# Kernel optimization log

Hardware: AMD Instinct MI355X
Metric: run time of the kernel (lower is better)

## Reference

```python
import jax, jax.numpy as jnp
import numpy as np

N = 100000
E = 1600000
F_IN = 128
HID = 64
N_CLASS = 40
NEG_SLOPE = 0.2


def setup_inputs() -> dict:
    key = jax.random.key(0)
    ks = jax.random.split(key, 16)
    s = lambda *sh: 1.0 / np.sqrt(sh[0])
    inp = {
        "x": jax.random.normal(ks[0], (N, F_IN), dtype=jnp.float32),
        "edge_index": jax.random.randint(ks[1], (2, E), 0, N, dtype=jnp.int64),
        "W1": jax.random.normal(ks[2], (F_IN, HID), jnp.float32) * s(F_IN),
        "b1": jnp.zeros((HID,), jnp.float32),
        "Wc0": jax.random.normal(ks[3], (HID, HID), jnp.float32) * s(HID),
        "att_src0": jax.random.normal(ks[4], (HID,), jnp.float32) * s(HID),
        "att_dst0": jax.random.normal(ks[5], (HID,), jnp.float32) * s(HID),
        "bias0": jnp.zeros((HID,), jnp.float32),
        "Wc1": jax.random.normal(ks[6], (HID, HID), jnp.float32) * s(HID),
        "att_src1": jax.random.normal(ks[7], (HID,), jnp.float32) * s(HID),
        "att_dst1": jax.random.normal(ks[8], (HID,), jnp.float32) * s(HID),
        "bias1": jnp.zeros((HID,), jnp.float32),
        "W2": jax.random.normal(ks[9], (HID, N_CLASS), jnp.float32) * s(HID),
        "b2": jnp.zeros((N_CLASS,), jnp.float32),
    }
    return inp


def gat_conv(x, src, dst, W, att_src, att_dst, bias):
    # x: [N, Fin]; src/dst: [E'] (self-loops already appended)
    h = x @ W                                   # [N, Fout]
    a_s = h @ att_src                           # [N]
    a_d = h @ att_dst                           # [N]
    e = jax.nn.leaky_relu(a_s[src] + a_d[dst], NEG_SLOPE)   # [E']
    # segment softmax over edges grouped by destination node
    e_max = jax.ops.segment_max(e, dst, num_segments=N)     # every node has a self-loop
    ex = jnp.exp(e - e_max[dst])
    denom = jax.ops.segment_sum(ex, dst, num_segments=N)
    alpha = ex / (denom[dst] + 1e-16)                        # [E']
    out = jax.ops.segment_sum(h[src] * alpha[:, None], dst, num_segments=N)
    return out + bias


def reference(x, edge_index, W1, b1, Wc0, att_src0, att_dst0, bias0,
              Wc1, att_src1, att_dst1, bias1, W2, b2):
    # eval mode: dropout_adj and feature dropout are identity
    loop = jnp.arange(N, dtype=edge_index.dtype)
    src = jnp.concatenate([edge_index[0], loop])
    dst = jnp.concatenate([edge_index[1], loop])

    h = jax.nn.relu(x @ W1 + b1)
    h = gat_conv(h, src, dst, Wc0, att_src0, att_dst0, bias0)
    h = jax.nn.relu(h)
    h = gat_conv(h, src, dst, Wc1, att_src1, att_dst1, bias1)
    logits = h @ W2 + b2
    return jax.nn.log_softmax(logits, axis=-1)
```

## Files before the change

### kernel.cpp

```cpp
#include <hip/hip_runtime.h>

#define N_NODES 100000
#define N_EDGES 1600000
#define F_IN    128
#define HID     64
#define N_CLASS 40
#define NEG_SLOPE 0.2f
#define ET (N_EDGES + N_NODES)
#define ROW_BLOCKS ((N_NODES + 63) / 64)

#define NCB   7
#define CAP1  294912
#define BPC   144
#define NFB   782
#define CAPF  2624
#define NT1   ((ET + 2047) / 2048)

typedef __attribute__((ext_vector_type(8))) short bf16x8;
typedef __attribute__((ext_vector_type(4))) float f32x4;

__device__ __forceinline__ unsigned int f2bf(float f) {
    unsigned int u = __float_as_uint(f);
    return (u + 0x7fffu + ((u >> 16) & 1u)) >> 16;
}

__global__ __launch_bounds__(256) void k_prepw(const float* __restrict__ W1,
        const float* __restrict__ Wc0, const float* __restrict__ Wc1,
        unsigned short* __restrict__ Wt1, unsigned short* __restrict__ Wtc0,
        unsigned short* __restrict__ Wtc1) {
    int t = threadIdx.x;
    for (int i = t; i < F_IN * HID; i += 256) {
        int k = i >> 6, n = i & 63;
        Wt1[n * F_IN + k] = (unsigned short)f2bf(W1[i]);
    }
    for (int i = t; i < HID * HID; i += 256) {
        int k = i >> 6, n = i & 63;
        Wtc0[n * HID + k] = (unsigned short)f2bf(Wc0[i]);
        Wtc1[n * HID + k] = (unsigned short)f2bf(Wc1[i]);
    }
}

__global__ __launch_bounds__(256) void k_lin1(const float* __restrict__ x,
        const unsigned short* __restrict__ Wt1, const float* __restrict__ b1,
        unsigned short* __restrict__ h0b) {
    __shared__ float xs[4][16 * 68];
    int t = threadIdx.x;
    int lane = t & 63, w = t >> 6;
    int quad = lane >> 4, lr = lane & 15;
    int rowg0 = blockIdx.x * 64 + w * 16;

    bf16x8 bfr[4][4];
    #pragma unroll
    for (int kc = 0; kc < 4; ++kc)
        #pragma unroll
        for (int nt = 0; nt < 4; ++nt)
            bfr[kc][nt] = *(const bf16x8*)(Wt1 + (nt * 16 + lr) * F_IN
                                           + kc * 32 + quad * 8);
    f32x4 zero = {0.f, 0.f, 0.f, 0.f};
    f32x4 acc[4] = {zero, zero, zero, zero};

    int arow = rowg0 + lr; if (arow >= N_NODES) arow = N_NODES - 1;
    const float* ab = x + (size_t)arow * F_IN;
    #pragma unroll
    for (int kc = 0; kc < 4; ++kc) {
        const float* ap = ab + kc * 32 + quad * 8;
        float4 a0 = *(const float4*)ap;
        float4 a1 = *(const float4*)(ap + 4);
        union { bf16x8 v; unsigned int u[4]; } af;
        af.u[0] = f2bf(a0.x) | (f2bf(a0.y) << 16);
        af.u[1] = f2bf(a0.z) | (f2bf(a0.w) << 16);
        af.u[2] = f2bf(a1.x) | (f2bf(a1.y) << 16);
        af.u[3] = f2bf(a1.z) | (f2bf(a1.w) << 16);
        #pragma unroll
        for (int nt = 0; nt < 4; ++nt)
            acc[nt] = __builtin_amdgcn_mfma_f32_16x16x32_bf16(
                          af.v, bfr[kc][nt], acc[nt], 0, 0, 0);
    }
    #pragma unroll
    for (int nt = 0; nt < 4; ++nt) {
        float bv = b1[nt * 16 + lr];
        #pragma unroll
        for (int reg = 0; reg < 4; ++reg)
            xs[w][(quad * 4 + reg) * 68 + nt * 16 + lr] =
                fmaxf(acc[nt][reg] + bv, 0.f);
    }
    __syncthreads();
    #pragma unroll
    for (int j = 0; j < 2; ++j) {
        int task = j * 64 + lane;
        int r = task >> 3, g = task & 7;
        int grow = blockIdx.x * 64 + w * 16 + r;
        if (grow < N_NODES) {
            const float* p = xs[w] + r * 68 + g * 8;
            uint4 u;
            u.x = f2bf(p[0]) | (f2bf(p[1]) << 16);
            u.y = f2bf(p[2]) | (f2bf(p[3]) << 16);
            u.z = f2bf(p[4]) | (f2bf(p[5]) << 16);
            u.w = f2bf(p[6]) | (f2bf(p[7]) << 16);
            *(uint4*)(h0b + (size_t)grow * HID + g * 8) = u;
        }
    }
}

__global__ __launch_bounds__(256) void k_gemm_att(
        const unsigned short* __restrict__ hin,
        const unsigned short* __restrict__ Wt,
        const float* __restrict__ att_s, const float* __restrict__ att_d,
        unsigned short* __restrict__ hb, float* __restrict__ as_,
        float* __restrict__ ad_) {
    __shared__ float xs[4][16 * 68];
    int t = threadIdx.x;
    int lane = t & 63, w = t >> 6;
    int quad = lane >> 4, lr = lane & 15;
    int rowg0 = blockIdx.x * 64 + w * 16;

    bf16x8 bfr[2][4];
    #pragma unroll
    for (int kc = 0; kc < 2; ++kc)
        #pragma unroll
        for (int nt = 0; nt < 4; ++nt)
            bfr[kc][nt] = *(const bf16x8*)(Wt + (nt * 16 + lr) * HID
                                           + kc * 32 + quad * 8);
    f32x4 zero = {0.f, 0.f, 0.f, 0.f};
    f32x4 acc[4] = {zero, zero, zero, zero};

    int arow = rowg0 + lr; if (arow >= N_NODES) arow = N_NODES - 1;
    #pragma unroll
    for (int kc = 0; kc < 2; ++kc) {
        bf16x8 af = *(const bf16x8*)(hin + (size_t)arow * HID
                                     + kc * 32 + quad * 8);
        #pragma unroll
        for (int nt = 0; nt < 4; ++nt)
            acc[nt] = __builtin_amdgcn_mfma_f32_16x16x32_bf16(
                          af, bfr[kc][nt], acc[nt], 0, 0, 0);
    }
    float asv[4], adv[4];
    #pragma unroll
    for (int nt = 0; nt < 4; ++nt) {
        asv[nt] = att_s[nt * 16 + lr];
        adv[nt] = att_d[nt * 16 + lr];
    }
    #pragma unroll
    for (int reg = 0; reg < 4; ++reg) {
        float p1 = acc[0][reg] * asv[0] + acc[1][reg] * asv[1]
                 + acc[2][reg] * asv[2] + acc[3][reg] * asv[3];
        float p2 = acc[0][reg] * adv[0] + acc[1][reg] * adv[1]
                 + acc[2][reg] * adv[2] + acc[3][reg] * adv[3];
        #pragma unroll
        for (int off = 1; off < 16; off <<= 1) {
            p1 += __shfl_xor(p1, off, 64);
            p2 += __shfl_xor(p2, off, 64);
        }
        if (lr == 0) {
            int grow = rowg0 + quad * 4 + reg;
            if (grow < N_NODES) { as_[grow] = p1; ad_[grow] = p2; }
        }
    }
    #pragma unroll
    for (int nt = 0; nt < 4; ++nt)
        #pragma unroll
        for (int reg = 0; reg < 4; ++reg)
            xs[w][(quad * 4 + reg) * 68 + nt * 16 + lr] = acc[nt][reg];
    __syncthreads();
    #pragma unroll
    for (int j = 0; j < 2; ++j) {
        int task = j * 64 + lane;
        int r = task >> 3, g = task & 7;
        int grow = blockIdx.x * 64 + w * 16 + r;
        if (grow < N_NODES) {
            const float* p = xs[w] + r * 68 + g * 8;
            uint4 u;
            u.x = f2bf(p[0]) | (f2bf(p[1]) << 16);
            u.y = f2bf(p[2]) | (f2bf(p[3]) << 16);
            u.z = f2bf(p[4]) | (f2bf(p[5]) << 16);
            u.w = f2bf(p[6]) | (f2bf(p[7]) << 16);
            *(uint4*)(hb + (size_t)grow * HID + g * 8) = u;
        }
    }
}

__global__ __launch_bounds__(256) void k_part1(const int* __restrict__ ei,
        int* __restrict__ tail1, int2* __restrict__ buf1) {
    __shared__ int2 eb[2048];
    __shared__ int hist[NCB], lbase[NCB], loff[NCB], goff[NCB];
    int t = threadIdx.x;
    int tileBase = blockIdx.x * 2048;
    int total = ET - tileBase; if (total > 2048) total = 2048;
    if (t < NCB) hist[t] = 0;
    __syncthreads();

    int sr[8], dr[8];
    #pragma unroll
    for (int r = 0; r < 8; ++r) {
        int i = tileBase + r * 256 + t;
        int s = -1, d = -1;
        if (i < ET) {
            if (i < N_EDGES) { s = ei[i]; d = ei[N_EDGES + i]; }
            else             { s = d = i - N_EDGES; }
            atomicAdd(&hist[d >> 14], 1);
        }
        sr[r] = s; dr[r] = d;
    }
    __syncthreads();
    if (t == 0) {
        int run = 0;
        for (int b = 0; b < NCB; ++b) { lbase[b] = run; loff[b] = 0; run += hist[b]; }
    }
    __syncthreads();
    if (t < NCB && hist[t] > 0) goff[t] = atomicAdd(&tail1[t], hist[t]);
    #pragma unroll
    for (int r = 0; r < 8; ++r) {
        if (dr[r] >= 0) {
            int b = dr[r] >> 14;
            int p = lbase[b] + atomicAdd(&loff[b], 1);
            eb[p] = make_int2(sr[r], dr[r]);
        }
    }
    __syncthreads();
    for (int j = t; j < total; j += 256) {
        int2 e = eb[j];
        int b = e.y >> 14;
        buf1[(size_t)b * CAP1 + goff[b] + (j - lbase[b])] = e;
    }
}

__global__ __launch_bounds__(256) void k_part2(const int2* __restrict__ buf1,
        const int* __restrict__ tail1, int* __restrict__ fcnt,
        int2* __restrict__ buf2) {
    __shared__ int2 eb[2048];
    __shared__ int hist[128], lbase[128], loff[128], goff[128], sc[128];
    int t = threadIdx.x;
    int cb   = blockIdx.x / BPC;
    int tile = blockIdx.x % BPC;
    int n1 = tail1[cb];
    int base = tile * 2048;
    if (base >= n1) return;
    int total = n1 - base; if (total > 2048) total = 2048;
    if (t < 128) hist[t] = 0;
    __syncthreads();

    int sr[8], dr[8];
    #pragma unroll
    for (int r = 0; r < 8; ++r) {
        int i = base + r * 256 + t;
        int s = -1, d = -1;
        if (i < n1) {
            int2 e = buf1[(size_t)cb * CAP1 + i];
            s = e.x; d = e.y;
            atomicAdd(&hist[(d >> 7) & 127], 1);
        }
        sr[r] = s; dr[r] = d;
    }
    __syncthreads();
    if (t < 128) sc[t] = hist[t];
    __syncthreads();
    for (int off = 1; off < 128; off <<= 1) {
        int u = (t < 128 && t >= off) ? sc[t - off] : 0;
        __syncthreads();
        if (t < 128) sc[t] += u;
        __syncthreads();
    }
    if (t < 128) { lbase[t] = sc[t] - hist[t]; loff[t] = 0; }
    __syncthreads();
    if (t < 128 && hist[t] > 0)
        goff[t] = atomicAdd(&fcnt[cb * 128 + t], hist[t]);
    #pragma unroll
    for (int r = 0; r < 8; ++r) {
        if (dr[r] >= 0) {
            int f = (dr[r] >> 7) & 127;
            int p = lbase[f] + atomicAdd(&loff[f], 1);
            eb[p] = make_int2(sr[r], dr[r]);
        }
    }
    __syncthreads();
    for (int j = t; j < total; j += 256) {
        int2 e = eb[j];
        int f = (e.y >> 7) & 127;
        buf2[(size_t)(e.y >> 7) * CAPF + goff[f] + (j - lbase[f])] = e;
    }
}

__global__ __launch_bounds__(1024) void k_fscan(const int* __restrict__ fcnt,
        int* __restrict__ fbase, int* __restrict__ rowptr) {
    __shared__ int s[1024];
    int t = threadIdx.x;
    int v = (t < NFB) ? fcnt[t] : 0;
    s[t] = v;
    __syncthreads();
    for (int off = 1; off < 1024; off <<= 1) {
        int u = (t >= off) ? s[t - off] : 0;
        __syncthreads();
        s[t] += u;
        __syncthreads();
    }
    if (t < NFB) fbase[t] = s[t] - v;
    if (t == 0) rowptr[N_NODES] = ET;
}

__global__ __launch_bounds__(256) void k_part3(const int2* __restrict__ buf2,
        const int* __restrict__ fcnt, const int* __restrict__ fbase,
        int* __restrict__ rowptr, int* __restrict__ col) {
    __shared__ int2 eb[CAPF];
    __shared__ int cs[CAPF];
    __shared__ int hist[128], lbase[128], loff[128], sc[128];
    int t = threadIdx.x;
    int fb = blockIdx.x;
    int nF = fcnt[fb];
    int gb = fbase[fb];
    int dbase = fb * 128;
    if (t < 128) hist[t] = 0;
    __syncthreads();
    for (int j = t; j < nF; j += 256) {
        int2 e = buf2[(size_t)fb * CAPF + j];
        eb[j] = e;
        atomicAdd(&hist[e.y - dbase], 1);
    }
    __syncthreads();
    if (t < 128) sc[t] = hist[t];
    __syncthreads();
    for (int off = 1; off < 128; off <<= 1) {
        int u = (t < 128 && t >= off) ? sc[t - off] : 0;
        __syncthreads();
        if (t < 128) sc[t] += u;
        __syncthreads();
    }
    if (t < 128) { lbase[t] = sc[t] - hist[t]; loff[t] = 0; }
    __syncthreads();
    if (t < 128 && dbase + t < N_NODES) rowptr[dbase + t] = gb + lbase[t];
    for (int j = t; j < nF; j += 256) {
        int2 e = eb[j];
        int r = e.y - dbase;
        int p = lbase[r] + atomicAdd(&loff[r], 1);
        cs[p] = e.x;
    }
    __syncthreads();
    for (int j = t; j < nF; j += 256) col[gb + j] = cs[j];
}

template <bool RELU, bool BF16OUT>
__global__ __launch_bounds__(256) void k_gat_agg(const int* __restrict__ rowptr,
        const int* __restrict__ col, const unsigned short* __restrict__ hb,
        const float* __restrict__ as_, const float* __restrict__ ad_,
        const float* __restrict__ bias, unsigned short* __restrict__ outb,
        float* __restrict__ outf) {
    int lane = threadIdx.x & 63;
    int d = blockIdx.x * 4 + (threadIdx.x >> 6);
    if (d >= N_NODES) return;
    int slot = lane >> 4;
    int ch   = (lane & 15) * 4;
    int beg = rowptr[d], end = rowptr[d + 1];
    float add = ad_[d];
    float ax = 0.f, ay = 0.f, az = 0.f, aw = 0.f, den = 0.f;
    for (int c = beg; c < end; c += 64) {
        int n = end - c;
        int sj = 0; float wj = 0.f;
        if (lane < n) {
            sj = col[c + lane];
            float e = as_[sj] + add;
            e = (e > 0.f) ? e : NEG_SLOPE * e;
            wj = __expf(e);
        }
        int m = (n < 64) ? n : 64;
        int iters = (m + 3) >> 2;
        for (int j = 0; j < iters; ++j) {
            int sl = j * 4 + slot;
            int   s = __shfl(sj, sl, 64);
            float w = __shfl(wj, sl, 64);
            den += w;
            uint2 hv = *(const uint2*)(hb + (size_t)s * HID + ch);
            float h0 = __uint_as_float(hv.x << 16);
            float h1 = __uint_as_float(hv.x & 0xffff0000u);
            float h2 = __uint_as_float(hv.y << 16);
            float h3 = __uint_as_float(hv.y & 0xffff0000u);
            ax = fmaf(w, h0, ax);
            ay = fmaf(w, h1, ay);
            az = fmaf(w, h2, az);
            aw = fmaf(w, h3, aw);
        }
    }
    #pragma unroll
    for (int off = 16; off <= 32; off <<= 1) {
        ax  += __shfl_xor(ax,  off, 64);
        ay  += __shfl_xor(ay,  off, 64);
        az  += __shfl_xor(az,  off, 64);
        aw  += __shfl_xor(aw,  off, 64);
        den += __shfl_xor(den, off, 64);
    }
    if (slot == 0) {
        float inv = 1.f / (den + 1e-16f);
        const float4 bv = *(const float4*)(bias + ch);
        float4 o;
        o.x = ax * inv + bv.x;
        o.y = ay * inv + bv.y;
        o.z = az * inv + bv.z;
        o.w = aw * inv + bv.w;
        if (RELU) {
            o.x = fmaxf(o.x, 0.f); o.y = fmaxf(o.y, 0.f);
            o.z = fmaxf(o.z, 0.f); o.w = fmaxf(o.w, 0.f);
        }
        if (BF16OUT) {
            uint2 u;
            u.x = f2bf(o.x) | (f2bf(o.y) << 16);
            u.y = f2bf(o.z) | (f2bf(o.w) << 16);
            *(uint2*)(outb + (size_t)d * HID + ch) = u;
        } else {
            *(float4*)(outf + (size_t)d * HID + ch) = o;
        }
    }
}

__global__ __launch_bounds__(64) void k_final(const float* __restrict__ agg,
        const float* __restrict__ W2, const float* __restrict__ b2,
        float* __restrict__ out) {
    __shared__ float xs[64 * 68];
    int lane = threadIdx.x;
    int base = blockIdx.x * 64;
    int rem = N_NODES - base; if (rem > 64) rem = 64;

    #pragma unroll
    for (int j = 0; j < 16; ++j) {
        int idx = j * 64 + lane;
        int r   = idx >> 4;
        int c4  = idx & 15;
        int gr  = base + r; if (gr >= N_NODES) gr = N_NODES - 1;
        float4 v = *(const float4*)(agg + (size_t)gr * HID + c4 * 4);
        *(float4*)(xs + r * 68 + c4 * 4) = v;
    }
    __syncthreads();

    float acc[N_CLASS];
    #pragma unroll
    for (int c = 0; c < N_CLASS; ++c) acc[c] = b2[c];
    const float* xrow = xs + lane * 68;
    #pragma unroll 2
    for (int k4 = 0; k4 < 16; ++k4) {
        float4 xv = *(const float4*)(xrow + 4 * k4);
        int kb = 4 * k4 * N_CLASS;
        #pragma unroll
        for (int c = 0; c < N_CLASS; ++c) {
            acc[c] = fmaf(xv.x, W2[kb + c],               acc[c]);
            acc[c] = fmaf(xv.y, W2[kb + N_CLASS + c],     acc[c]);
            acc[c] = fmaf(xv.z, W2[kb + 2 * N_CLASS + c], acc[c]);
            acc[c] = fmaf(xv.w, W2[kb + 3 * N_CLASS + c], acc[c]);
        }
    }
    float m = acc[0];
    #pragma unroll
    for (int c = 1; c < N_CLASS; ++c) m = fmaxf(m, acc[c]);
    float ssum = 0.f;
    #pragma unroll
    for (int c = 0; c < N_CLASS; ++c) ssum += __expf(acc[c] - m);
    float lse = m + logf(ssum);

    __syncthreads();
    #pragma unroll
    for (int c4 = 0; c4 < 10; ++c4) {
        float4 o;
        o.x = acc[4 * c4 + 0] - lse; o.y = acc[4 * c4 + 1] - lse;
        o.z = acc[4 * c4 + 2] - lse; o.w = acc[4 * c4 + 3] - lse;
        *(float4*)(xs + lane * N_CLASS + c4 * 4) = o;
    }
    __syncthreads();
    #pragma unroll
    for (int j = 0; j < 10; ++j) {
        int idx = j * 64 + lane;
        if (idx < rem * 10) {
            float4 v = *(const float4*)(xs + idx * 4);
            *(float4*)(out + (size_t)base * N_CLASS + idx * 4) = v;
        }
    }
}

extern "C" void kernel_launch(void* const* d_in, const int* in_sizes, int n_in,
                              void* d_out, int out_size, void* d_ws, size_t ws_size,
                              hipStream_t stream) {
    const float* x     = (const float*)d_in[0];
    const int*   ei    = (const int*)  d_in[1];
    const float* W1    = (const float*)d_in[2];
    const float* b1    = (const float*)d_in[3];
    const float* Wc0   = (const float*)d_in[4];
    const float* as0   = (const float*)d_in[5];
    const float* ad0   = (const float*)d_in[6];
    const float* bias0 = (const float*)d_in[7];
    const float* Wc1   = (const float*)d_in[8];
    const float* as1   = (const float*)d_in[9];
    const float* ad1   = (const float*)d_in[10];
    const float* bias1 = (const float*)d_in[11];
    const float* W2    = (const float*)d_in[12];
    const float* b2    = (const float*)d_in[13];
    float* out = (float*)d_out;

    char* base = (char*)d_ws;
    char* R1 = base;
    char* R2 = base + (size_t)N_NODES * HID * 4;
    unsigned short* h0b  = (unsigned short*)R1;
    float*          agg1 = (float*)R1;
    int2*           buf2 = (int2*)R1;
    unsigned short* hb   = (unsigned short*)R2;
    unsigned short* agg0b = (unsigned short*)(R2 + (size_t)N_NODES * HID * 2);
    int2*           buf1 = (int2*)R2;

    char* mp = R2 + (size_t)N_NODES * HID * 4;
    unsigned short* Wt1  = (unsigned short*)mp;  mp += F_IN * HID * 2;
    unsigned short* Wtc0 = (unsigned short*)mp;  mp += HID * HID * 2;
    unsigned short* Wtc1 = (unsigned short*)mp;  mp += HID * HID * 2;
    float* as_   = (float*)mp;                   mp += N_NODES * 4;
    float* ad_   = (float*)mp;                   mp += N_NODES * 4;
    int*   col   = (int*)mp;                     mp += (size_t)ET * 4;
    int*   tail1 = (int*)mp;                     mp += NCB * 4;
    int*   fcnt  = (int*)mp;                     mp += NFB * 4;
    int*   fbase = (int*)mp;                     mp += NFB * 4;
    int*   rowptr= (int*)mp;

    const int AGG_BLOCKS = (N_NODES + 3) / 4;

    hipMemsetAsync(tail1, 0, (NCB + NFB) * sizeof(int), stream);
    k_prepw<<<1, 256, 0, stream>>>(W1, Wc0, Wc1, Wt1, Wtc0, Wtc1);
    k_part1<<<NT1, 256, 0, stream>>>(ei, tail1, buf1);
    k_part2<<<NCB * BPC, 256, 0, stream>>>(buf1, tail1, fcnt, buf2);
    k_fscan<<<1, 1024, 0, stream>>>(fcnt, fbase, rowptr);
    k_part3<<<NFB, 256, 0, stream>>>(buf2, fcnt, fbase, rowptr, col);

    k_lin1<<<ROW_BLOCKS, 256, 0, stream>>>(x, Wt1, b1, h0b);

    k_gemm_att<<<ROW_BLOCKS, 256, 0, stream>>>(h0b, Wtc0, as0, ad0,
                                               hb, as_, ad_);
    k_gat_agg<true, true><<<AGG_BLOCKS, 256, 0, stream>>>(
        rowptr, col, hb, as_, ad_, bias0, agg0b, (float*)nullptr);

    k_gemm_att<<<ROW_BLOCKS, 256, 0, stream>>>(agg0b, Wtc1, as1, ad1,
                                               hb, as_, ad_);
    k_gat_agg<false, false><<<AGG_BLOCKS, 256, 0, stream>>>(
        rowptr, col, hb, as_, ad_, bias1, (unsigned short*)nullptr, agg1);

    k_final<<<ROW_BLOCKS, 64, 0, stream>>>(agg1, W2, b2, out);
}
```

Measured before the change: 347.2 us.

## Degree-sort nodes for 8-lane-per-node GAT aggregation and MFMA final layer

Adds a degree histogram, scan and scatter that order nodes by in-degree. The aggregation kernel then packs 8 nodes per wavefront, with 8 lanes per node and 8 channels per lane, so work per wave is balanced and fewer lanes sit idle. The second layer's output is now written as bf16, and the final linear layer plus log-softmax runs on bf16 MFMA using a pre-transposed, zero-padded W2. In exchange it adds three small kernels and atomic contention on a 64-bin histogram, and the bf16 intermediate and bf16 W2 lower precision.

```diff
diff --git a/kernel.cpp b/kernel.cpp
--- a/kernel.cpp
+++ b/kernel.cpp
@@ -26,8 +26,9 @@
 
 __global__ __launch_bounds__(256) void k_prepw(const float* __restrict__ W1,
         const float* __restrict__ Wc0, const float* __restrict__ Wc1,
+        const float* __restrict__ W2,
         unsigned short* __restrict__ Wt1, unsigned short* __restrict__ Wtc0,
-        unsigned short* __restrict__ Wtc1) {
+        unsigned short* __restrict__ Wtc1, unsigned short* __restrict__ W2t) {
     int t = threadIdx.x;
     for (int i = t; i < F_IN * HID; i += 256) {
         int k = i >> 6, n = i & 63;
@@ -37,6 +38,11 @@
         int k = i >> 6, n = i & 63;
         Wtc0[n * HID + k] = (unsigned short)f2bf(Wc0[i]);
         Wtc1[n * HID + k] = (unsigned short)f2bf(Wc1[i]);
+    }
+    for (int i = t; i < 48 * HID; i += 256) {
+        int n = i >> 6, k = i & 63;
+        W2t[n * HID + k] = (n < N_CLASS)
+            ? (unsigned short)f2bf(W2[k * N_CLASS + n]) : (unsigned short)0;
     }
 }
 
@@ -337,135 +343,170 @@
     for (int j = t; j < nF; j += 256) col[gb + j] = cs[j];
 }
 
-template <bool RELU, bool BF16OUT>
+__global__ __launch_bounds__(256) void k_dhist(const int* __restrict__ rowptr,
+        int* __restrict__ dhist) {
+    int i = blockIdx.x * 256 + threadIdx.x;
+    if (i >= N_NODES) return;
+    int deg = rowptr[i + 1] - rowptr[i];
+    if (deg > 63) deg = 63;
+    atomicAdd(&dhist[deg], 1);
+}
+
+__global__ __launch_bounds__(64) void k_dscan(const int* __restrict__ dhist,
+        int* __restrict__ dbase) {
+    int t = threadIdx.x;
+    int v = dhist[t];
+    int s = v;
+    #pragma unroll
+    for (int off = 1; off < 64; off <<= 1) {
+        int u = __shfl_up(s, off, 64);
+        if (t >= off) s += u;
+    }
+    dbase[t] = s - v;
+}
+
+__global__ __launch_bounds__(256) void k_dscatter(const int* __restrict__ rowptr,
+        int* __restrict__ dbase, int* __restrict__ nodeord) {
+    int i = blockIdx.x * 256 + threadIdx.x;
+    if (i >= N_NODES) return;
+    int deg = rowptr[i + 1] - rowptr[i];
+    if (deg > 63) deg = 63;
+    int pos = atomicAdd(&dbase[deg], 1);
+    nodeord[pos] = i;
+}
+
+template <bool RELU>
 __global__ __launch_bounds__(256) void k_gat_agg(const int* __restrict__ rowptr,
         const int* __restrict__ col, const unsigned short* __restrict__ hb,
         const float* __restrict__ as_, const float* __restrict__ ad_,
-        const float* __restrict__ bias, unsigned short* __restrict__ outb,
-        float* __restrict__ outf) {
-    int lane = threadIdx.x & 63;
-    int d = blockIdx.x * 4 + (threadIdx.x >> 6);
-    if (d >= N_NODES) return;
-    int slot = lane >> 4;
-    int ch   = (lane & 15) * 4;
-    int beg = rowptr[d], end = rowptr[d + 1];
+        const float* __restrict__ bias, const int* __restrict__ nodeord,
+        unsigned short* __restrict__ outb) {
+    int t = threadIdx.x;
+    int lane = t & 63;
+    int wid = blockIdx.x * 4 + (t >> 6);
+    int l8 = lane & 7;
+    int ch = l8 * 8;
+    int d = nodeord[wid * 8 + (lane >> 3)];
+    int beg = rowptr[d];
+    int deg = rowptr[d + 1] - beg;
     float add = ad_[d];
-    float ax = 0.f, ay = 0.f, az = 0.f, aw = 0.f, den = 0.f;
-    for (int c = beg; c < end; c += 64) {
-        int n = end - c;
+    int degw = deg;
+    degw = max(degw, __shfl_xor(degw, 8, 64));
+    degw = max(degw, __shfl_xor(degw, 16, 64));
+    degw = max(degw, __shfl_xor(degw, 32, 64));
+
+    float a0=0.f,a1=0.f,a2=0.f,a3=0.f,a4=0.f,a5=0.f,a6=0.f,a7=0.f,den=0.f;
+    const unsigned short* hch = hb + ch;
+    for (int c = 0; c < degw; c += 8) {
+        int idx = c + l8;
         int sj = 0; float wj = 0.f;
-        if (lane < n) {
-            sj = col[c + lane];
+        if (idx < deg) {
+            sj = col[beg + idx];
             float e = as_[sj] + add;
             e = (e > 0.f) ? e : NEG_SLOPE * e;
             wj = __expf(e);
         }
-        int m = (n < 64) ? n : 64;
-        int iters = (m + 3) >> 2;
-        for (int j = 0; j < iters; ++j) {
-            int sl = j * 4 + slot;
-            int   s = __shfl(sj, sl, 64);
-            float w = __shfl(wj, sl, 64);
-            den += w;
-            uint2 hv = *(const uint2*)(hb + (size_t)s * HID + ch);
-            float h0 = __uint_as_float(hv.x << 16);
-            float h1 = __uint_as_float(hv.x & 0xffff0000u);
-            float h2 = __uint_as_float(hv.y << 16);
-            float h3 = __uint_as_float(hv.y & 0xffff0000u);
-            ax = fmaf(w, h0, ax);
-            ay = fmaf(w, h1, ay);
-            az = fmaf(w, h2, az);
-            aw = fmaf(w, h3, aw);
-        }
-    }
-    #pragma unroll
-    for (int off = 16; off <= 32; off <<= 1) {
-        ax  += __shfl_xor(ax,  off, 64);
-        ay  += __shfl_xor(ay,  off, 64);
-        az  += __shfl_xor(az,  off, 64);
-        aw  += __shfl_xor(aw,  off, 64);
-        den += __shfl_xor(den, off, 64);
-    }
-    if (slot == 0) {
-        float inv = 1.f / (den + 1e-16f);
-        const float4 bv = *(const float4*)(bias + ch);
-        float4 o;
-        o.x = ax * inv + bv.x;
-        o.y = ay * inv + bv.y;
-        o.z = az * inv + bv.z;
-        o.w = aw * inv + bv.w;
-        if (RELU) {
-            o.x = fmaxf(o.x, 0.f); o.y = fmaxf(o.y, 0.f);
-            o.z = fmaxf(o.z, 0.f); o.w = fmaxf(o.w, 0.f);
-        }
-        if (BF16OUT) {
-            uint2 u;
-            u.x = f2bf(o.x) | (f2bf(o.y) << 16);
-            u.y = f2bf(o.z) | (f2bf(o.w) << 16);
-            *(uint2*)(outb + (size_t)d * HID + ch) = u;
-        } else {
-            *(float4*)(outf + (size_t)d * HID + ch) = o;
-        }
-    }
-}
-
-__global__ __launch_bounds__(64) void k_final(const float* __restrict__ agg,
-        const float* __restrict__ W2, const float* __restrict__ b2,
+        #pragma unroll
+        for (int j = 0; j < 8; ++j) {
+            int sl = (lane & 56) | j;
+            int   s  = __shfl(sj, sl, 64);
+            float w0 = __shfl(wj, sl, 64);
+            den += w0;
+            uint4 hv = *(const uint4*)(hch + (size_t)s * HID);
+            a0 = fmaf(w0, __uint_as_float(hv.x << 16),         a0);
+            a1 = fmaf(w0, __uint_as_float(hv.x & 0xffff0000u), a1);
+            a2 = fmaf(w0, __uint_as_float(hv.y << 16),         a2);
+            a3 = fmaf(w0, __uint_as_float(hv.y & 0xffff0000u), a3);
+            a4 = fmaf(w0, __uint_as_float(hv.z << 16),         a4);
+            a5 = fmaf(w0, __uint_as_float(hv.z & 0xffff0000u), a5);
+            a6 = fmaf(w0, __uint_as_float(hv.w << 16),         a6);
+            a7 = fmaf(w0, __uint_as_float(hv.w & 0xffff0000u), a7);
+        }
+    }
+    float inv = 1.f / (den + 1e-16f);
+    float4 bA = *(const float4*)(bias + ch);
+    float4 bB = *(const float4*)(bias + ch + 4);
+    float o0 = fmaf(a0, inv, bA.x), o1 = fmaf(a1, inv, bA.y);
+    float o2 = fmaf(a2, inv, bA.z), o3 = fmaf(a3, inv, bA.w);
+    float o4 = fmaf(a4, inv, bB.x), o5 = fmaf(a5, inv, bB.y);
+    float o6 = fmaf(a6, inv, bB.z), o7 = fmaf(a7, inv, bB.w);
+    if (RELU) {
+        o0 = fmaxf(o0, 0.f); o1 = fmaxf(o1, 0.f);
+        o2 = fmaxf(o2, 0.f); o3 = fmaxf(o3, 0.f);
+        o4 = fmaxf(o4, 0.f); o5 = fmaxf(o5, 0.f);
+        o6 = fmaxf(o6, 0.f); o7 = fmaxf(o7, 0.f);
+    }
+    uint4 u;
+    u.x = f2bf(o0) | (f2bf(o1) << 16);
+    u.y = f2bf(o2) | (f2bf(o3) << 16);
+    u.z = f2bf(o4) | (f2bf(o5) << 16);
+    u.w = f2bf(o6) | (f2bf(o7) << 16);
+    *(uint4*)(outb + (size_t)d * HID + ch) = u;
+}
+
+__global__ __launch_bounds__(256) void k_final(
+        const unsigned short* __restrict__ aggb,
+        const unsigned short* __restrict__ W2t, const float* __restrict__ b2,
         float* __restrict__ out) {
-    __shared__ float xs[64 * 68];
-    int lane = threadIdx.x;
+    __shared__ float xs[64 * 44];
+    int t = threadIdx.x;
+    int lane = t & 63, w = t >> 6;
+    int quad = lane >> 4, lr = lane & 15;
+    int rowg0 = blockIdx.x * 64 + w * 16;
     int base = blockIdx.x * 64;
     int rem = N_NODES - base; if (rem > 64) rem = 64;
 
-    #pragma unroll
-    for (int j = 0; j < 16; ++j) {
-        int idx = j * 64 + lane;
-        int r   = idx >> 4;
-        int c4  = idx & 15;
-        int gr  = base + r; if (gr >= N_NODES) gr = N_NODES - 1;
-        float4 v = *(const float4*)(agg + (size_t)gr * HID + c4 * 4);
-        *(float4*)(xs + r * 68 + c4 * 4) = v;
-    }
-    __syncthreads();
-
-    float acc[N_CLASS];
-    #pragma unroll
-    for (int c = 0; c < N_CLASS; ++c) acc[c] = b2[c];
-    const float* xrow = xs + lane * 68;
-    #pragma unroll 2
-    for (int k4 = 0; k4 < 16; ++k4) {
-        float4 xv = *(const float4*)(xrow + 4 * k4);
-        int kb = 4 * k4 * N_CLASS;
-        #pragma unroll
-        for (int c = 0; c < N_CLASS; ++c) {
-            acc[c] = fmaf(xv.x, W2[kb + c],               acc[c]);
-            acc[c] = fmaf(xv.y, W2[kb + N_CLASS + c],     acc[c]);
-            acc[c] = fmaf(xv.z, W2[kb + 2 * N_CLASS + c], acc[c]);
-            acc[c] = fmaf(xv.w, W2[kb + 3 * N_CLASS + c], acc[c]);
-        }
-    }
-    float m = acc[0];
-    #pragma unroll
-    for (int c = 1; c < N_CLASS; ++c) m = fmaxf(m, acc[c]);
-    float ssum = 0.f;
-    #pragma unroll
-    for (int c = 0; c < N_CLASS; ++c) ssum += __expf(acc[c] - m);
-    float lse = m + logf(ssum);
-
-    __syncthreads();
-    #pragma unroll
-    for (int c4 = 0; c4 < 10; ++c4) {
-        float4 o;
-        o.x = acc[4 * c4 + 0] - lse; o.y = acc[4 * c4 + 1] - lse;
-        o.z = acc[4 * c4 + 2] - lse; o.w = acc[4 * c4 + 3] - lse;
-        *(float4*)(xs + lane * N_CLASS + c4 * 4) = o;
-    }
-    __syncthreads();
-    #pragma unroll
-    for (int j = 0; j < 10; ++j) {
-        int idx = j * 64 + lane;
+    bf16x8 bfr[2][3];
+    #pragma unroll
+    for (int kc = 0; kc < 2; ++kc)
+        #pragma unroll
+        for (int nt = 0; nt < 3; ++nt)
+            bfr[kc][nt] = *(const bf16x8*)(W2t + (nt * 16 + lr) * HID
+                                           + kc * 32 + quad * 8);
+    f32x4 zero = {0.f, 0.f, 0.f, 0.f};
+    f32x4 acc[3] = {zero, zero, zero};
+    int arow = rowg0 + lr; if (arow >= N_NODES) arow = N_NODES - 1;
+    #pragma unroll
+    for (int kc = 0; kc < 2; ++kc) {
+        bf16x8 af = *(const bf16x8*)(aggb + (size_t)arow * HID
+                                     + kc * 32 + quad * 8);
+        #pragma unroll
+        for (int nt = 0; nt < 3; ++nt)
+            acc[nt] = __builtin_amdgcn_mfma_f32_16x16x32_bf16(
+                          af, bfr[kc][nt], acc[nt], 0, 0, 0);
+    }
+    float bc[3];
+    #pragma unroll
+    for (int nt = 0; nt < 3; ++nt) {
+        int cl = nt * 16 + lr;
+        bc[nt] = (cl < N_CLASS) ? b2[cl] : -1e30f;
+    }
+    #pragma unroll
+    for (int reg = 0; reg < 4; ++reg) {
+        float v0 = acc[0][reg] + bc[0];
+        float v1 = acc[1][reg] + bc[1];
+        float v2 = acc[2][reg] + bc[2];
+        float m = fmaxf(fmaxf(v0, v1), v2);
+        #pragma unroll
+        for (int off = 1; off < 16; off <<= 1)
+            m = fmaxf(m, __shfl_xor(m, off, 64));
+        float ss = __expf(v0 - m) + __expf(v1 - m) + __expf(v2 - m);
+        #pragma unroll
+        for (int off = 1; off < 16; off <<= 1)
+            ss += __shfl_xor(ss, off, 64);
+        float lse = m + logf(ss);
+        int r = w * 16 + quad * 4 + reg;
+        xs[r * 44 + lr]      = v0 - lse;
+        xs[r * 44 + 16 + lr] = v1 - lse;
+        if (lr < 8) xs[r * 44 + 32 + lr] = v2 - lse;
+    }
+    __syncthreads();
+    #pragma unroll
+    for (int j = 0; j < 3; ++j) {
+        int idx = j * 256 + t;
         if (idx < rem * 10) {
-            float4 v = *(const float4*)(xs + idx * 4);
+            int r = idx / 10, c4 = idx - r * 10;
+            float4 v = *(const float4*)(xs + r * 44 + c4 * 4);
             *(float4*)(out + (size_t)base * N_CLASS + idx * 4) = v;
         }
     }
@@ -490,48 +531,56 @@
     const float* b2    = (const float*)d_in[13];
     float* out = (float*)d_out;
 
-    char* base = (char*)d_ws;
-    char* R1 = base;
-    char* R2 = base + (size_t)N_NODES * HID * 4;
-    unsigned short* h0b  = (unsigned short*)R1;
-    float*          agg1 = (float*)R1;
-    int2*           buf2 = (int2*)R1;
-    unsigned short* hb   = (unsigned short*)R2;
+    char* basep = (char*)d_ws;
+    char* R1 = basep;
+    char* R2 = basep + (size_t)N_NODES * HID * 4;
+    unsigned short* h0b   = (unsigned short*)R1;
+    unsigned short* agg1b = (unsigned short*)R1;
+    int*            nodeord = (int*)(R1 + (size_t)N_NODES * HID * 2);
+    int2*           buf2  = (int2*)R1;
+    unsigned short* hb    = (unsigned short*)R2;
     unsigned short* agg0b = (unsigned short*)(R2 + (size_t)N_NODES * HID * 2);
-    int2*           buf1 = (int2*)R2;
+    int2*           buf1  = (int2*)R2;
 
     char* mp = R2 + (size_t)N_NODES * HID * 4;
     unsigned short* Wt1  = (unsigned short*)mp;  mp += F_IN * HID * 2;
     unsigned short* Wtc0 = (unsigned short*)mp;  mp += HID * HID * 2;
     unsigned short* Wtc1 = (unsigned short*)mp;  mp += HID * HID * 2;
+    unsigned short* W2t  = (unsigned short*)mp;  mp += 48 * HID * 2;
     float* as_   = (float*)mp;                   mp += N_NODES * 4;
     float* ad_   = (float*)mp;                   mp += N_NODES * 4;
     int*   col   = (int*)mp;                     mp += (size_t)ET * 4;
     int*   tail1 = (int*)mp;                     mp += NCB * 4;
     int*   fcnt  = (int*)mp;                     mp += NFB * 4;
     int*   fbase = (int*)mp;                     mp += NFB * 4;
+    int*   dhist = (int*)mp;                     mp += 64 * 4;
+    int*   dbase = (int*)mp;                     mp += 64 * 4;
     int*   rowptr= (int*)mp;
 
-    const int AGG_BLOCKS = (N_NODES + 3) / 4;
-
-    hipMemsetAsync(tail1, 0, (NCB + NFB) * sizeof(int), stream);
-    k_prepw<<<1, 256, 0, stream>>>(W1, Wc0, Wc1, Wt1, Wtc0, Wtc1);
+    const int AGG_BLOCKS = N_NODES / 32;
+    const int NODE_BLOCKS = (N_NODES + 255) / 256;
+
+    hipMemsetAsync(tail1, 0, (NCB + 2 * NFB + 128) * sizeof(int), stream);
+    k_prepw<<<1, 256, 0, stream>>>(W1, Wc0, Wc1, W2, Wt1, Wtc0, Wtc1, W2t);
     k_part1<<<NT1, 256, 0, stream>>>(ei, tail1, buf1);
     k_part2<<<NCB * BPC, 256, 0, stream>>>(buf1, tail1, fcnt, buf2);
     k_fscan<<<1, 1024, 0, stream>>>(fcnt, fbase, rowptr);
     k_part3<<<NFB, 256, 0, stream>>>(buf2, fcnt, fbase, rowptr, col);
+    k_dhist<<<NODE_BLOCKS, 256, 0, stream>>>(rowptr, dhist);
+    k_dscan<<<1, 64, 0, stream>>>(dhist, dbase);
+    k_dscatter<<<NODE_BLOCKS, 256, 0, stream>>>(rowptr, dbase, nodeord);
 
     k_lin1<<<ROW_BLOCKS, 256, 0, stream>>>(x, Wt1, b1, h0b);
 
     k_gemm_att<<<ROW_BLOCKS, 256, 0, stream>>>(h0b, Wtc0, as0, ad0,
                                                hb, as_, ad_);
-    k_gat_agg<true, true><<<AGG_BLOCKS, 256, 0, stream>>>(
-        rowptr, col, hb, as_, ad_, bias0, agg0b, (float*)nullptr);
+    k_gat_agg<true><<<AGG_BLOCKS, 256, 0, stream>>>(
+        rowptr, col, hb, as_, ad_, bias0, nodeord, agg0b);
 
     k_gemm_att<<<ROW_BLOCKS, 256, 0, stream>>>(agg0b, Wtc1, as1, ad1,
                                                hb, as_, ad_);
-    k_gat_agg<false, false><<<AGG_BLOCKS, 256, 0, stream>>>(
-        rowptr, col, hb, as_, ad_, bias1, (unsigned short*)nullptr, agg1);
-
-    k_final<<<ROW_BLOCKS, 64, 0, stream>>>(agg1, W2, b2, out);
-}
+    k_gat_agg<false><<<AGG_BLOCKS, 256, 0, stream>>>(
+        rowptr, col, hb, as_, ad_, bias1, nodeord, agg1b);
+
+    k_final<<<ROW_BLOCKS, 256, 0, stream>>>(agg1b, W2t, b2, out);
+}
```

Result: slower. 887.8 us (+155.7%).
